# Kernel optimization log

Measured on AMD Instinct MI355X. Metric: run time of the kernel, lower is better.

## Reference

```python
import jax, jax.numpy as jnp
import numpy as np

K_FRAC = 0.5  # init arg k (keep fraction)


def setup_inputs() -> dict:
    key = jax.random.key(0)
    k1, k2, k3, k4, k5 = jax.random.split(key, 5)
    B, N, F = 1, 100000, 128
    E, Fe = 1600000, 32
    x = jax.random.normal(k1, (B, N, F), jnp.float32)
    edge_index = jax.random.randint(k2, (2, E), 0, N, dtype=jnp.int32)
    edge_attr = jax.random.normal(k3, (B, E, Fe), jnp.float32)
    # nn.Linear(in_dim, 1) params
    proj_w = jax.random.normal(k4, (1, F), jnp.float32) / jnp.sqrt(F)
    proj_b = jax.random.normal(k5, (1,), jnp.float32) * 0.01
    return {"x": x, "edge_attr": edge_attr, "proj_w": proj_w,
            "proj_b": proj_b, "edge_index": edge_index}


def reference(x, edge_attr, proj_w, proj_b, edge_index):
    B, N, F = x.shape
    # linear score + sigmoid (dropout p=0 -> identity)
    scores = jax.nn.sigmoid(jnp.einsum('bnf,of->bno', x, proj_w)[..., 0] + proj_b[0])  # [B,N]
    # torch.kthvalue(scores, kth, dim=1): kth smallest (1-indexed)
    kth = int((1.0 - K_FRAC) * N)
    kth_scores = jnp.sort(scores, axis=1)[:, kth - 1:kth]  # [B,1]
    mask = scores >= kth_scores  # [B,N]
    n_keep = int(N * K_FRAC)
    # stable descending sort of mask.float() -> true indices first, in original order
    pool_indices = jnp.argsort(jnp.where(mask, 0, 1), axis=1)[:, :n_keep]  # [B,n_keep]
    new_x = jnp.take_along_axis(x, pool_indices[..., None], axis=1)  # [B,n_keep,F]
    # 1-D node mask shared across batch (as in the torch code)
    node_mask = jnp.zeros((N,), bool).at[pool_indices].set(True)
    pool_edges = node_mask[edge_index[0]] & node_mask[edge_index[1]]  # [E] bool
    new_edge_index = edge_index[:, pool_edges]        # [2, E'] (data-dependent, eager)
    new_edge_attr = edge_attr[:, pool_edges]          # [B, E', Fe]
    mapping = jnp.full((N,), -1, jnp.int32).at[pool_indices].set(
        jnp.broadcast_to(jnp.arange(n_keep, dtype=jnp.int32), pool_indices.shape))
    new_edge_index_ordered = mapping[new_edge_index]
    return (new_x, new_edge_index, new_edge_index_ordered, new_edge_attr,
            pool_indices, pool_edges)
```

## Files before the change

### kernel.cpp

```cpp
#include <hip/hip_runtime.h>
#include <math.h>

#define ST_AGG 1ull
#define ST_PRE 2ull

__global__ __launch_bounds__(256) void scores_hist_kernel(
    const float* __restrict__ x, const float* __restrict__ w,
    const float* __restrict__ bptr, int N, int F, unsigned* __restrict__ scores,
    unsigned* __restrict__ hist) {
  __shared__ float tX[64 * 128];
  __shared__ double sPart[4 * 64];
  __shared__ float wS[128];
  int t = threadIdx.x;
  int blockBase = blockIdx.x * 256;
  if (t < 128) wS[t] = w[t];
  __syncthreads();
  int row = t & 63, seg = t >> 6;
  float4 wreg[8];
  {
    const float4* w4 = (const float4*)(wS + seg * 32);
    #pragma unroll
    for (int k = 0; k < 8; k++) wreg[k] = w4[k];
  }
  double bias = (double)bptr[0];
  for (int tile = 0; tile < 4; tile++) {
    int rowBase = blockBase + tile * 64;
    {
      const float4* src = (const float4*)(x + (size_t)rowBase * 128);
      float4* dst = (float4*)tX;
      #pragma unroll
      for (int k = 0; k < 8; k++) {
        int idx = t + k * 256;
        int grow = rowBase + (idx >> 5);
        float4 v = make_float4(0.f, 0.f, 0.f, 0.f);
        if (grow < N) v = src[idx];
        dst[idx] = v;
      }
    }
    __syncthreads();
    {
      const float4* xr = (const float4*)(tX + row * 128 + seg * 32);
      double acc = 0.0;
      #pragma unroll
      for (int k = 0; k < 8; k++) {
        float4 xv = xr[k];
        float4 wv = wreg[k];
        acc += (double)xv.x * (double)wv.x;
        acc += (double)xv.y * (double)wv.y;
        acc += (double)xv.z * (double)wv.z;
        acc += (double)xv.w * (double)wv.w;
      }
      sPart[seg * 64 + row] = acc;
    }
    __syncthreads();
    if (t < 64) {
      int node = rowBase + t;
      if (node < N) {
        double z = sPart[t] + sPart[64 + t] + sPart[128 + t] + sPart[192 + t] + bias;
        double s = 1.0 / (1.0 + exp(-z));
        unsigned bits = __float_as_uint((float)s);
        scores[node] = bits;
        atomicAdd(&hist[bits >> 16], 1u);
      }
    }
    __syncthreads();
  }
}

__global__ __launch_bounds__(256) void hist2_kernel(
    const unsigned* __restrict__ scores, int N, const unsigned* __restrict__ sel,
    unsigned* __restrict__ hist) {
  int i = blockIdx.x * 256 + threadIdx.x;
  if (i >= N) return;
  unsigned bits = scores[i];
  if ((bits >> 16) == sel[0]) atomicAdd(&hist[bits & 0xFFFFu], 1u);
}

__global__ __launch_bounds__(256) void select_kernel(
    const unsigned* __restrict__ hist, const unsigned* __restrict__ qptr, unsigned qconst,
    unsigned* __restrict__ outB, unsigned* __restrict__ outRem) {
  __shared__ unsigned tot[256];
  __shared__ unsigned bins[256];
  __shared__ unsigned sChunk, sRem;
  int t = threadIdx.x;
  unsigned q = qptr ? *qptr : qconst;
  const uint4* hp = (const uint4*)(hist + t * 256);
  unsigned s = 0;
  #pragma unroll 8
  for (int j = 0; j < 64; j++) {
    uint4 v = hp[j];
    s += v.x + v.y + v.z + v.w;
  }
  tot[t] = s;
  __syncthreads();
  if (t == 0) {
    unsigned cum = 0; int c = 0;
    for (; c < 256; c++) { if (q < cum + tot[c]) break; cum += tot[c]; }
    sChunk = (unsigned)c; sRem = q - cum;
  }
  __syncthreads();
  bins[t] = hist[sChunk * 256 + t];
  __syncthreads();
  if (t == 0) {
    unsigned cum = 0; unsigned q2 = sRem; int bi = 0;
    for (; bi < 256; bi++) { if (q2 < cum + bins[bi]) break; cum += bins[bi]; }
    *outB = sChunk * 256 + bi;
    *outRem = q2 - cum;
  }
}

__device__ __forceinline__ unsigned lookback_exclusive(
    unsigned long long* status, int bid, int lane) {
  unsigned excl = 0;
  int j = bid - 1;
  for (;;) {
    int idx = j - lane;
    unsigned long long st;
    if (idx >= 0) {
      do {
        st = __hip_atomic_load(&status[idx], __ATOMIC_RELAXED, __HIP_MEMORY_SCOPE_AGENT);
      } while ((st >> 32) == 0ull);
    } else {
      st = (ST_PRE << 32);
    }
    int isPre = ((st >> 32) == ST_PRE);
    unsigned long long preb = __ballot(isPre);
    int p = __ffsll(preb) - 1;
    unsigned contrib = (p < 0 || lane <= p) ? (unsigned)st : 0u;
    for (int off = 32; off > 0; off >>= 1)
      contrib += __shfl_down(contrib, off, 64);
    excl += __shfl(contrib, 0, 64);
    if (p >= 0) return excl;
    j -= 64;
  }
}

__device__ __forceinline__ void publish_status(
    unsigned long long* status, int bid, unsigned long long st, unsigned v) {
  __hip_atomic_store(&status[bid], (st << 32) | (unsigned long long)v,
                     __ATOMIC_RELAXED, __HIP_MEMORY_SCOPE_AGENT);
}

__global__ __launch_bounds__(256) void node_compact(
    const unsigned* __restrict__ scores, const unsigned* __restrict__ sel,
    const float* __restrict__ x, int N, int F, int n_keep,
    unsigned* __restrict__ ticket, unsigned long long* __restrict__ status,
    int* __restrict__ map, float* __restrict__ out_pool, float* __restrict__ outx) {
  __shared__ unsigned sBid;
  __shared__ unsigned wv[4];
  __shared__ unsigned sExcl;
  __shared__ int sSrc[256];
  int t = threadIdx.x;
  if (t == 0) sBid = atomicAdd(ticket, 1u);
  __syncthreads();
  int bid = (int)sBid;
  int i = bid * 256 + t;
  unsigned T = (sel[0] << 16) | sel[2];
  int m = (i < N) && (scores[i] >= T);
  unsigned long long bal = __ballot(m);
  int lane = t & 63, wave = t >> 6;
  if (lane == 0) wv[wave] = (unsigned)__popcll(bal);
  __syncthreads();
  unsigned agg = wv[0] + wv[1] + wv[2] + wv[3];
  if (wave == 0) {
    if (lane == 0 && bid > 0) publish_status(status, bid, ST_AGG, agg);
    unsigned excl = (bid > 0) ? lookback_exclusive(status, bid, lane) : 0u;
    if (lane == 0) {
      publish_status(status, bid, ST_PRE, excl + agg);
      sExcl = excl;
    }
  }
  __syncthreads();
  unsigned wpre = 0;
  for (int k = 0; k < wave; k++) wpre += wv[k];
  unsigned li = wpre + (unsigned)__popcll(bal & ((1ull << lane) - 1ull));
  if (i < N) {
    int mv = -1;
    if (m) {
      unsigned pre = sExcl + li;
      if (pre < (unsigned)n_keep) {
        mv = (int)pre;
        out_pool[pre] = (float)i;
        sSrc[li] = i;
      }
    }
    map[i] = mv;
  }
  __syncthreads();
  unsigned lim = agg;
  if (sExcl + agg > (unsigned)n_keep)
    lim = ((unsigned)n_keep > sExcl) ? ((unsigned)n_keep - sExcl) : 0u;
  for (int k = t >> 5; k < (int)lim; k += 8) {
    const float4* s4 = (const float4*)(x + (size_t)sSrc[k] * F);
    float4* d4 = (float4*)(outx + (size_t)(sExcl + (unsigned)k) * F);
    d4[t & 31] = s4[t & 31];
  }
}

__global__ __launch_bounds__(256) void edge_compact(
    const int* __restrict__ ei, const int* __restrict__ map, int E, int Ek, int Fe,
    const float* __restrict__ attr,
    unsigned* __restrict__ ticket, unsigned long long* __restrict__ status,
    float* __restrict__ out,
    size_t o_ei, size_t o_eio, size_t o_attr, size_t o_pe) {
  __shared__ unsigned sBid;
  __shared__ unsigned wv[4];
  __shared__ unsigned sExcl;
  __shared__ int sE[1024];
  int t = threadIdx.x;
  if (t == 0) sBid = atomicAdd(ticket, 1u);
  __syncthreads();
  int bid = (int)sBid;
  int e0 = bid * 1024 + t * 4;
  int m[4] = {0, 0, 0, 0};
  int av[4], bv[4], mav[4], mbv[4];
  unsigned c = 0;
  if (e0 < E) {
    int4 a4 = ((const int4*)ei)[(size_t)bid * 256 + t];
    int4 b4 = ((const int4*)(ei + E))[(size_t)bid * 256 + t];
    av[0] = a4.x; av[1] = a4.y; av[2] = a4.z; av[3] = a4.w;
    bv[0] = b4.x; bv[1] = b4.y; bv[2] = b4.z; bv[3] = b4.w;
    #pragma unroll
    for (int j = 0; j < 4; j++) {
      mav[j] = map[av[j]];
      mbv[j] = map[bv[j]];
      m[j] = (mav[j] >= 0) && (mbv[j] >= 0);
      c += (unsigned)m[j];
    }
    float4 pe4 = make_float4((float)m[0], (float)m[1], (float)m[2], (float)m[3]);
    *(float4*)(out + o_pe + e0) = pe4;
  }
  int lane = t & 63, wave = t >> 6;
  unsigned incl = c;
  #pragma unroll
  for (int off = 1; off < 64; off <<= 1) {
    unsigned u = __shfl_up(incl, off, 64);
    if (lane >= off) incl += u;
  }
  if (lane == 63) wv[wave] = incl;
  __syncthreads();
  unsigned agg = wv[0] + wv[1] + wv[2] + wv[3];
  if (wave == 0) {
    if (lane == 0 && bid > 0) publish_status(status, bid, ST_AGG, agg);
    unsigned excl = (bid > 0) ? lookback_exclusive(status, bid, lane) : 0u;
    if (lane == 0) {
      publish_status(status, bid, ST_PRE, excl + agg);
      sExcl = excl;
    }
  }
  __syncthreads();
  unsigned wpre = 0;
  for (int k = 0; k < wave; k++) wpre += wv[k];
  unsigned li = wpre + (incl - c);
  if (e0 < E) {
    unsigned r = li;
    #pragma unroll
    for (int j = 0; j < 4; j++) {
      if (m[j]) {
        unsigned p = sExcl + r;
        out[o_ei + p]              = (float)av[j];
        out[o_ei + (size_t)Ek + p] = (float)bv[j];
        out[o_eio + p]              = (float)mav[j];
        out[o_eio + (size_t)Ek + p] = (float)mbv[j];
        sE[r] = e0 + j;
        r++;
      }
    }
  }
  __syncthreads();
  for (int k = t >> 3; k < (int)agg; k += 32) {
    const float4* src = (const float4*)(attr + (size_t)sE[k] * Fe);
    float4* dst = (float4*)(out + o_attr + (size_t)(sExcl + (unsigned)k) * Fe);
    dst[t & 7] = src[t & 7];
  }
}

extern "C" void kernel_launch(void* const* d_in, const int* in_sizes, int n_in,
                              void* d_out, int out_size, void* d_ws, size_t ws_size,
                              hipStream_t stream) {
  const int F  = in_sizes[2];
  const int E  = in_sizes[4] / 2;
  const int N  = in_sizes[0] / F;
  const int Fe = in_sizes[1] / E;
  const int n_keep = N / 2;
  const unsigned q = (unsigned)(N - n_keep - 1);
  const int Ek = (int)(((long long)out_size - (long long)n_keep * F - n_keep - E) / (4 + Fe));

  const float* x    = (const float*)d_in[0];
  const float* attr = (const float*)d_in[1];
  const float* w    = (const float*)d_in[2];
  const float* b    = (const float*)d_in[3];
  const int*   ei   = (const int*)d_in[4];
  float*       out  = (float*)d_out;

  const size_t o_newx = 0;
  const size_t o_ei   = (size_t)n_keep * F;
  const size_t o_eio  = o_ei + 2 * (size_t)Ek;
  const size_t o_attr = o_eio + 2 * (size_t)Ek;
  const size_t o_pool = o_attr + (size_t)Ek * Fe;
  const size_t o_pe   = o_pool + (size_t)n_keep;

  char* wsb = (char*)d_ws;
  size_t off = 0;
  auto carve = [&](size_t bytes) -> void* {
    void* p = wsb + off;
    off = (off + bytes + 255) & ~(size_t)255;
    return p;
  };
  const int nb_n  = (N + 255) / 256;
  const int nb_e  = (E + 1023) / 1024;
  unsigned* scores = (unsigned*)carve((size_t)N * 4);
  size_t zero_begin = off;
  unsigned* hist1   = (unsigned*)carve((size_t)65536 * 4);
  unsigned* hist2   = (unsigned*)carve((size_t)65536 * 4);
  unsigned* tickets = (unsigned*)carve(2 * 4);
  unsigned long long* status_n = (unsigned long long*)carve((size_t)nb_n * 8);
  unsigned long long* status_e = (unsigned long long*)carve((size_t)nb_e * 8);
  size_t zero_end = off;
  unsigned* sel    = (unsigned*)carve(64);
  int* map         = (int*)carve((size_t)N * 4);
  (void)ws_size;

  hipMemsetAsync(hist1, 0, zero_end - zero_begin, stream);
  scores_hist_kernel<<<nb_n, 256, 0, stream>>>(x, w, b, N, F, scores, hist1);
  select_kernel<<<1, 256, 0, stream>>>(hist1, nullptr, q, sel + 0, sel + 1);
  hist2_kernel<<<nb_n, 256, 0, stream>>>(scores, N, sel, hist2);
  select_kernel<<<1, 256, 0, stream>>>(hist2, sel + 1, 0u, sel + 2, sel + 3);
  node_compact<<<nb_n, 256, 0, stream>>>(scores, sel, x, N, F, n_keep, tickets + 0,
                                         status_n, map, out + o_pool, out + o_newx);
  edge_compact<<<nb_e, 256, 0, stream>>>(ei, map, E, Ek, Fe, attr, tickets + 1, status_e,
                                         out, o_ei, o_eio, o_attr, o_pe);
}
```

Measured before the change: 485.9 us.

## Fuse radix-select into histogram kernels via last-block pattern and stage edge writes in LDS

After: 522.0 us. +7.4%, slower.

```diff
diff --git a/kernel.cpp b/kernel.cpp
--- a/kernel.cpp
+++ b/kernel.cpp
@@ -3,14 +3,66 @@
 
 #define ST_AGG 1ull
 #define ST_PRE 2ull
+
+__device__ __forceinline__ void block_select(
+    const unsigned* __restrict__ hist, unsigned q,
+    unsigned* __restrict__ outB, unsigned* __restrict__ outRem) {
+  __shared__ unsigned sc[256];
+  __shared__ unsigned sres[2];
+  int t = threadIdx.x;
+  {
+    const unsigned long long* hp = (const unsigned long long*)(hist + t * 256);
+    unsigned s = 0;
+    #pragma unroll 8
+    for (int j = 0; j < 128; j++) {
+      unsigned long long v =
+          __hip_atomic_load(&hp[j], __ATOMIC_RELAXED, __HIP_MEMORY_SCOPE_AGENT);
+      s += (unsigned)v + (unsigned)(v >> 32);
+    }
+    sc[t] = s;
+    unsigned val = s;
+    __syncthreads();
+    for (int st = 1; st < 256; st <<= 1) {
+      unsigned a = (t >= st) ? sc[t - st] : 0u;
+      __syncthreads();
+      sc[t] += a;
+      __syncthreads();
+    }
+    unsigned incl = sc[t], excl = incl - val;
+    if (q >= excl && q < incl) { sres[0] = (unsigned)t; sres[1] = q - excl; }
+  }
+  __syncthreads();
+  unsigned chunk = sres[0], rem = sres[1];
+  {
+    unsigned v = __hip_atomic_load(&hist[chunk * 256 + t], __ATOMIC_RELAXED,
+                                   __HIP_MEMORY_SCOPE_AGENT);
+    __syncthreads();
+    sc[t] = v;
+    unsigned val = v;
+    __syncthreads();
+    for (int st = 1; st < 256; st <<= 1) {
+      unsigned a = (t >= st) ? sc[t - st] : 0u;
+      __syncthreads();
+      sc[t] += a;
+      __syncthreads();
+    }
+    unsigned incl = sc[t], excl = incl - val;
+    if (rem >= excl && rem < incl) {
+      *outB = chunk * 256 + t;
+      *outRem = rem - excl;
+    }
+  }
+}
 
 __global__ __launch_bounds__(256) void scores_hist_kernel(
     const float* __restrict__ x, const float* __restrict__ w,
     const float* __restrict__ bptr, int N, int F, unsigned* __restrict__ scores,
-    unsigned* __restrict__ hist) {
+    unsigned* __restrict__ hist, unsigned qconst, unsigned* __restrict__ sel,
+    unsigned* __restrict__ doneCnt) {
   __shared__ float tX[64 * 128];
   __shared__ double sPart[4 * 64];
   __shared__ float wS[128];
+  __shared__ unsigned sLast;
   int t = threadIdx.x;
   int blockBase = blockIdx.x * 256;
   if (t < 128) wS[t] = w[t];
@@ -65,48 +117,26 @@
     }
     __syncthreads();
   }
+  __threadfence();
+  if (t == 0) sLast = (atomicAdd(doneCnt, 1u) == gridDim.x - 1u) ? 1u : 0u;
+  __syncthreads();
+  if (sLast) block_select(hist, qconst, sel + 0, sel + 1);
 }
 
 __global__ __launch_bounds__(256) void hist2_kernel(
     const unsigned* __restrict__ scores, int N, const unsigned* __restrict__ sel,
-    unsigned* __restrict__ hist) {
+    unsigned* __restrict__ hist, unsigned* __restrict__ selOut,
+    unsigned* __restrict__ doneCnt) {
+  __shared__ unsigned sLast;
   int i = blockIdx.x * 256 + threadIdx.x;
-  if (i >= N) return;
-  unsigned bits = scores[i];
-  if ((bits >> 16) == sel[0]) atomicAdd(&hist[bits & 0xFFFFu], 1u);
-}
-
-__global__ __launch_bounds__(256) void select_kernel(
-    const unsigned* __restrict__ hist, const unsigned* __restrict__ qptr, unsigned qconst,
-    unsigned* __restrict__ outB, unsigned* __restrict__ outRem) {
-  __shared__ unsigned tot[256];
-  __shared__ unsigned bins[256];
-  __shared__ unsigned sChunk, sRem;
-  int t = threadIdx.x;
-  unsigned q = qptr ? *qptr : qconst;
-  const uint4* hp = (const uint4*)(hist + t * 256);
-  unsigned s = 0;
-  #pragma unroll 8
-  for (int j = 0; j < 64; j++) {
-    uint4 v = hp[j];
-    s += v.x + v.y + v.z + v.w;
-  }
-  tot[t] = s;
-  __syncthreads();
-  if (t == 0) {
-    unsigned cum = 0; int c = 0;
-    for (; c < 256; c++) { if (q < cum + tot[c]) break; cum += tot[c]; }
-    sChunk = (unsigned)c; sRem = q - cum;
-  }
-  __syncthreads();
-  bins[t] = hist[sChunk * 256 + t];
-  __syncthreads();
-  if (t == 0) {
-    unsigned cum = 0; unsigned q2 = sRem; int bi = 0;
-    for (; bi < 256; bi++) { if (q2 < cum + bins[bi]) break; cum += bins[bi]; }
-    *outB = sChunk * 256 + bi;
-    *outRem = q2 - cum;
-  }
+  if (i < N) {
+    unsigned bits = scores[i];
+    if ((bits >> 16) == sel[0]) atomicAdd(&hist[bits & 0xFFFFu], 1u);
+  }
+  __threadfence();
+  if (threadIdx.x == 0) sLast = (atomicAdd(doneCnt, 1u) == gridDim.x - 1u) ? 1u : 0u;
+  __syncthreads();
+  if (sLast) block_select(hist, sel[1], selOut + 0, selOut + 1);
 }
 
 __device__ __forceinline__ unsigned lookback_exclusive(
@@ -207,6 +237,7 @@
   __shared__ unsigned wv[4];
   __shared__ unsigned sExcl;
   __shared__ int sE[1024];
+  __shared__ float sA[1024], sB[1024], sMA[1024], sMB[1024];
   int t = threadIdx.x;
   if (t == 0) sBid = atomicAdd(ticket, 1u);
   __syncthreads();
@@ -251,23 +282,28 @@
   __syncthreads();
   unsigned wpre = 0;
   for (int k = 0; k < wave; k++) wpre += wv[k];
-  unsigned li = wpre + (incl - c);
+  unsigned r = wpre + (incl - c);
   if (e0 < E) {
-    unsigned r = li;
     #pragma unroll
     for (int j = 0; j < 4; j++) {
       if (m[j]) {
-        unsigned p = sExcl + r;
-        out[o_ei + p]              = (float)av[j];
-        out[o_ei + (size_t)Ek + p] = (float)bv[j];
-        out[o_eio + p]              = (float)mav[j];
-        out[o_eio + (size_t)Ek + p] = (float)mbv[j];
-        sE[r] = e0 + j;
+        sE[r]  = e0 + j;
+        sA[r]  = (float)av[j];
+        sB[r]  = (float)bv[j];
+        sMA[r] = (float)mav[j];
+        sMB[r] = (float)mbv[j];
         r++;
       }
     }
   }
   __syncthreads();
+  for (int k = t; k < (int)agg; k += 256) {
+    unsigned p = sExcl + (unsigned)k;
+    out[o_ei + p]              = sA[k];
+    out[o_ei + (size_t)Ek + p] = sB[k];
+    out[o_eio + p]              = sMA[k];
+    out[o_eio + (size_t)Ek + p] = sMB[k];
+  }
   for (int k = t >> 3; k < (int)agg; k += 32) {
     const float4* src = (const float4*)(attr + (size_t)sE[k] * Fe);
     float4* dst = (float4*)(out + o_attr + (size_t)(sExcl + (unsigned)k) * Fe);
@@ -313,7 +349,7 @@
   size_t zero_begin = off;
   unsigned* hist1   = (unsigned*)carve((size_t)65536 * 4);
   unsigned* hist2   = (unsigned*)carve((size_t)65536 * 4);
-  unsigned* tickets = (unsigned*)carve(2 * 4);
+  unsigned* tickets = (unsigned*)carve(4 * 4);
   unsigned long long* status_n = (unsigned long long*)carve((size_t)nb_n * 8);
   unsigned long long* status_e = (unsigned long long*)carve((size_t)nb_e * 8);
   size_t zero_end = off;
@@ -322,10 +358,9 @@
   (void)ws_size;
 
   hipMemsetAsync(hist1, 0, zero_end - zero_begin, stream);
-  scores_hist_kernel<<<nb_n, 256, 0, stream>>>(x, w, b, N, F, scores, hist1);
-  select_kernel<<<1, 256, 0, stream>>>(hist1, nullptr, q, sel + 0, sel + 1);
-  hist2_kernel<<<nb_n, 256, 0, stream>>>(scores, N, sel, hist2);
-  select_kernel<<<1, 256, 0, stream>>>(hist2, sel + 1, 0u, sel + 2, sel + 3);
+  scores_hist_kernel<<<nb_n, 256, 0, stream>>>(x, w, b, N, F, scores, hist1,
+                                               q, sel, tickets + 2);
+  hist2_kernel<<<nb_n, 256, 0, stream>>>(scores, N, sel, hist2, sel + 2, tickets + 3);
   node_compact<<<nb_n, 256, 0, stream>>>(scores, sel, x, N, F, n_keep, tickets + 0,
                                          status_n, map, out + o_pool, out + o_newx);
   edge_compact<<<nb_e, 256, 0, stream>>>(ei, map, E, Ek, Fe, attr, tickets + 1, status_e,
```
